# Optimization experiments

Hardware: AMD Instinct MI355X
Metric: run time of the kernel (lower is better)

The kernel has to match this reference:

```python
import jax, jax.numpy as jnp
import numpy as np

PF = 57     # player_features
TL = 35     # team_length (hardcoded in call)
EXTRA = 6   # trailing features x[:, :, 206:]
B, T = 64, 1024
D_IN = TL + 3 * PF + EXTRA          # 212
FEAT = 5 + 3 * 10 + EXTRA           # 41 (team_embed 5 + player_embed 30 + extra)
H = 256                             # LSTM units


def setup_inputs() -> dict:
    key = jax.random.key(0)
    ks = jax.random.split(key, 24)
    w = lambda k, shp, s=0.05: (jax.random.normal(k, shp, jnp.float32) * s)
    z = lambda n: jnp.zeros((n,), jnp.float32)
    return {
        "x": jax.random.normal(ks[0], (B, T, D_IN), jnp.float32),
        # encoder_player: Dense(57->27, relu), Dense(27->10, relu)
        "pe_w1": w(ks[1], (PF, 27)), "pe_b1": z(27),
        "pe_w2": w(ks[2], (27, 10)), "pe_b2": z(10),
        # encoder_team: Dense(35->17, relu), Dense(17->5, relu)
        "te_w1": w(ks[3], (TL, 17)), "te_b1": z(17),
        "te_w2": w(ks[4], (17, 5)),  "te_b2": z(5),
        # stacked LSTMs (keras kernel layout [in,4H] gate order i,f,c,o)
        "W1": w(ks[5], (FEAT, 4 * H)), "U1": w(ks[6], (H, 4 * H)), "bl1": z(4 * H),
        "W2": w(ks[7], (H, 4 * H)),    "U2": w(ks[8], (H, 4 * H)), "bl2": z(4 * H),
        "W3": w(ks[9], (H, 4 * H)),    "U3": w(ks[10], (H, 4 * H)), "bl3": z(4 * H),
        # head: Dense(256->100 relu), Dense(100->40 relu), Dense(40->2 softmax)
        "d1w": w(ks[11], (H, 100)), "d1b": z(100),
        "d2w": w(ks[12], (100, 40)), "d2b": z(40),
        "d3w": w(ks[13], (40, 2)),  "d3b": z(2),
    }


def _lstm_softmax(x, W, U, b):
    """Keras LSTM with activation=softmax, recurrent_activation=sigmoid.
    x: [B,T,D] -> hidden sequence [B,T,H]."""
    xz = jnp.einsum('btd,dk->btk', x, W) + b          # precompute input projection [B,T,4H]
    h0 = jnp.zeros((x.shape[0], U.shape[0]), x.dtype)

    def step(carry, xt):
        h, c = carry
        zt = xt + h @ U                               # [B,4H]
        i, f, g, o = jnp.split(zt, 4, axis=-1)        # keras gate order i,f,c,o
        c = jax.nn.sigmoid(f) * c + jax.nn.sigmoid(i) * jax.nn.softmax(g, axis=-1)
        h = jax.nn.sigmoid(o) * jax.nn.softmax(c, axis=-1)
        return (h, c), h

    _, hs = jax.lax.scan(step, (h0, h0), jnp.swapaxes(xz, 0, 1))
    return jnp.swapaxes(hs, 0, 1)


def reference(x, pe_w1, pe_b1, pe_w2, pe_b2, te_w1, te_b1, te_w2, te_b2,
              W1, U1, bl1, W2, U2, bl2, W3, U3, bl3,
              d1w, d1b, d2w, d2b, d3w, d3b):
    Bn, Tn = x.shape[0], x.shape[1]
    relu = jax.nn.relu

    # team encoder
    team = x[:, :, :TL].reshape(-1, TL)
    te = relu(relu(team @ te_w1 + te_b1) @ te_w2 + te_b2).reshape(Bn, Tn, -1)  # [B,T,5]

    # player encoder: shooter/assister/blocker rows concatenated then re-flattened
    s = x[:, :, TL:TL + PF].reshape(-1, PF)
    a = x[:, :, TL + PF:TL + 2 * PF].reshape(-1, PF)
    bk = x[:, :, TL + 2 * PF:TL + 3 * PF].reshape(-1, PF)
    players = jnp.concatenate([s, a, bk], axis=1).reshape(-1, PF)              # [3BT,57]
    pe = relu(relu(players @ pe_w1 + pe_b1) @ pe_w2 + pe_b2).reshape(Bn, Tn, -1)  # [B,T,30]

    # faithful out-of-range slices (clamp like TF strided_slice):
    shooter_e = pe[:, :, :PF]                  # whole 30 dims
    assister_e = pe[:, :, PF:2 * PF]           # empty [B,T,0]
    blocker_e = pe[:, :, 2 * PF:]              # empty [B,T,0]

    feat = jnp.concatenate(
        [te, shooter_e, assister_e, blocker_e, x[:, :, TL + 3 * PF:]], axis=2)  # [B,T,41]

    h = _lstm_softmax(feat, W1, U1, bl1)
    h = _lstm_softmax(h, W2, U2, bl2)
    h_last = _lstm_softmax(h, W3, U3, bl3)[:, -1]                               # [B,256]

    out = relu(h_last @ d1w + d1b)
    out = relu(out @ d2w + d2b)
    return jax.nn.softmax(out @ d3w + d3b, axis=-1)                             # [B,2]
```

## Files before the change

kernel.cpp:

```cpp
#include <hip/hip_runtime.h>

typedef _Float16 f16;
typedef _Float16 h2 __attribute__((ext_vector_type(2)));
typedef float f32x2 __attribute__((ext_vector_type(2)));

#define NBATCH 64
#define TSTEPS 1024
#define NH 256
#define FSTR 44

#define OFF_FEAT 0ull
#define OFF_XZ   11534336ull
#define OFF_H    145752064ull
#define OFF_UPK  179306496ull

#define QLDS 18
#define QALL 32
#define QSTR (QALL - QLDS)
#define SMEM_SCAN8 (QLDS * 1024 * 8 + 1024 + 4096 + 64)

__device__ __forceinline__ float sigmf(float z) {
  return 1.f / (1.f + __expf(-z));
}

__device__ __forceinline__ float wave_sum64(float v) {
#pragma unroll
  for (int off = 32; off; off >>= 1) v += __shfl_xor(v, off);
  return v;
}

__device__ __forceinline__ void fp8x4_mac(unsigned w, float4 hv,
                                          float& a0, float& a1) {
  f32x2 lo = __builtin_amdgcn_cvt_pk_f32_fp8(w, false);
  f32x2 hi = __builtin_amdgcn_cvt_pk_f32_fp8(w, true);
  a0 = fmaf(lo.x, hv.x, a0);
  a1 = fmaf(lo.y, hv.y, a1);
  a0 = fmaf(hi.x, hv.z, a0);
  a1 = fmaf(hi.y, hv.w, a1);
}

__global__ __launch_bounds__(256) void cvt_u_fp8(const float* __restrict__ U,
                                                 uint2* __restrict__ dst) {
  int id = blockIdx.x * 256 + threadIdx.x;
  int q = id >> 10, c = id & 1023;
  unsigned vx = 0, vy = 0;
  vx = __builtin_amdgcn_cvt_pk_fp8_f32(U[(8 * q + 0) * 1024 + c],
                                       U[(8 * q + 1) * 1024 + c], vx, false);
  vx = __builtin_amdgcn_cvt_pk_fp8_f32(U[(8 * q + 2) * 1024 + c],
                                       U[(8 * q + 3) * 1024 + c], vx, true);
  vy = __builtin_amdgcn_cvt_pk_fp8_f32(U[(8 * q + 4) * 1024 + c],
                                       U[(8 * q + 5) * 1024 + c], vy, false);
  vy = __builtin_amdgcn_cvt_pk_fp8_f32(U[(8 * q + 6) * 1024 + c],
                                       U[(8 * q + 7) * 1024 + c], vy, true);
  dst[id] = uint2{vx, vy};
}

__global__ __launch_bounds__(256) void embed_feat(
    const float* __restrict__ x,
    const float* __restrict__ pe_w1, const float* __restrict__ pe_b1,
    const float* __restrict__ pe_w2, const float* __restrict__ pe_b2,
    const float* __restrict__ te_w1, const float* __restrict__ te_b1,
    const float* __restrict__ te_w2, const float* __restrict__ te_b2,
    float* __restrict__ feat) {
  __shared__ float w[2548];
  const int tid = threadIdx.x;
  for (int i = tid; i < 595; i += 256) w[i] = te_w1[i];
  for (int i = tid; i < 17; i += 256) w[595 + i] = te_b1[i];
  for (int i = tid; i < 85; i += 256) w[612 + i] = te_w2[i];
  for (int i = tid; i < 5; i += 256) w[697 + i] = te_b2[i];
  for (int i = tid; i < 1539; i += 256) w[702 + i] = pe_w1[i];
  for (int i = tid; i < 27; i += 256) w[2241 + i] = pe_b1[i];
  for (int i = tid; i < 270; i += 256) w[2268 + i] = pe_w2[i];
  for (int i = tid; i < 10; i += 256) w[2538 + i] = pe_b2[i];
  __syncthreads();

  int row = blockIdx.x * 256 + tid;
  const float* xr = x + (size_t)row * 212;
  float* fr = feat + (size_t)row * FSTR;

  {
    float h1[17];
#pragma unroll
    for (int h = 0; h < 17; ++h) h1[h] = w[595 + h];
    for (int k = 0; k < 35; ++k) {
      float xv = xr[k];
#pragma unroll
      for (int h = 0; h < 17; ++h) h1[h] += xv * w[k * 17 + h];
    }
#pragma unroll
    for (int h = 0; h < 17; ++h) h1[h] = fmaxf(h1[h], 0.f);
    float t2[5];
#pragma unroll
    for (int h = 0; h < 5; ++h) t2[h] = w[697 + h];
#pragma unroll
    for (int k = 0; k < 17; ++k) {
#pragma unroll
      for (int h = 0; h < 5; ++h) t2[h] += h1[k] * w[612 + k * 5 + h];
    }
#pragma unroll
    for (int h = 0; h < 5; ++h) fr[h] = fmaxf(t2[h], 0.f);
  }
  for (int p = 0; p < 3; ++p) {
    const float* xp = xr + 35 + 57 * p;
    float h1[27];
#pragma unroll
    for (int h = 0; h < 27; ++h) h1[h] = w[2241 + h];
    for (int k = 0; k < 57; ++k) {
      float xv = xp[k];
#pragma unroll
      for (int h = 0; h < 27; ++h) h1[h] += xv * w[702 + k * 27 + h];
    }
#pragma unroll
    for (int h = 0; h < 27; ++h) h1[h] = fmaxf(h1[h], 0.f);
    float t2[10];
#pragma unroll
    for (int h = 0; h < 10; ++h) t2[h] = w[2538 + h];
#pragma unroll
    for (int k = 0; k < 27; ++k) {
#pragma unroll
      for (int h = 0; h < 10; ++h) t2[h] += h1[k] * w[2268 + k * 10 + h];
    }
#pragma unroll
    for (int h = 0; h < 10; ++h) fr[5 + 10 * p + h] = fmaxf(t2[h], 0.f);
  }
#pragma unroll
  for (int e = 0; e < 6; ++e) fr[35 + e] = xr[206 + e];
}

__global__ __launch_bounds__(256) void gemm_feat(
    const float* __restrict__ feat, const float* __restrict__ W,
    const float* __restrict__ bias, f16* __restrict__ C) {
  __shared__ float Wl[41 * 256];
  __shared__ float fl[64 * FSTR];
  int m0 = blockIdx.x * 64, n0 = blockIdx.y * 256;
  int t = threadIdx.x;
  for (int r = 0; r < 41; ++r) Wl[r * 256 + t] = W[r * 1024 + n0 + t];
  for (int i = t; i < 64 * FSTR; i += 256) fl[i] = feat[(size_t)m0 * FSTR + i];
  __syncthreads();
  float bv = bias[n0 + t];
  for (int r = 0; r < 64; ++r) {
    float acc = bv;
#pragma unroll
    for (int k = 0; k < 41; ++k) acc += fl[r * FSTR + k] * Wl[k * 256 + t];
    C[(size_t)(m0 + r) * 1024 + n0 + t] = (f16)acc;
  }
}

__global__ __launch_bounds__(256) void gemm_h(
    const f16* __restrict__ A, const float* __restrict__ B,
    const float* __restrict__ bias, f16* __restrict__ C) {
  __shared__ float As[32][72];
  __shared__ float Bs[32][64];
  int m0 = blockIdx.x * 64, n0 = blockIdx.y * 64;
  int t = threadIdx.x;
  int tx = t & 15, ty = t >> 4;
  float acc[4][4];
#pragma unroll
  for (int i = 0; i < 4; ++i)
#pragma unroll
    for (int j = 0; j < 4; ++j) acc[i][j] = 0.f;

  float bcol[4];
#pragma unroll
  for (int j = 0; j < 4; ++j) bcol[j] = bias[n0 + tx * 4 + j];

  for (int k0 = 0; k0 < 256; k0 += 32) {
    {
      int r = t >> 2, kq = (t & 3) * 8;
      const f16* ap = A + (size_t)(m0 + r) * 256 + k0 + kq;
      float4 raw = *(const float4*)ap;
      const f16* hv = (const f16*)&raw;
#pragma unroll
      for (int q = 0; q < 8; ++q) As[kq + q][r] = (float)hv[q];
    }
    {
      int kr = t >> 3, nq = (t & 7) * 8;
      const float* bp = B + (size_t)(k0 + kr) * 1024 + n0 + nq;
      float4 b0 = *(const float4*)bp;
      float4 b1 = *(const float4*)(bp + 4);
      *(float4*)&Bs[kr][nq] = b0;
      *(float4*)&Bs[kr][nq + 4] = b1;
    }
    __syncthreads();
#pragma unroll
    for (int kk = 0; kk < 32; ++kk) {
      float4 av = *(const float4*)&As[kk][ty * 4];
      float4 bv = *(const float4*)&Bs[kk][tx * 4];
      const float* ap = (const float*)&av;
      const float* bp = (const float*)&bv;
#pragma unroll
      for (int i = 0; i < 4; ++i)
#pragma unroll
        for (int j = 0; j < 4; ++j) acc[i][j] += ap[i] * bp[j];
    }
    __syncthreads();
  }
#pragma unroll
  for (int i = 0; i < 4; ++i) {
    int row = m0 + ty * 4 + i;
    alignas(8) f16 ov[4];
#pragma unroll
    for (int j = 0; j < 4; ++j) ov[j] = (f16)(acc[i][j] + bcol[j]);
    *(uint2*)(C + (size_t)row * 1024 + n0 + tx * 4) = *(const uint2*)ov;
  }
}

__global__ __launch_bounds__(512) void lstm_scan_f8(
    const uint2* __restrict__ Wall,
    const f16* __restrict__ xz,
    f16* __restrict__ hseq) {
  extern __shared__ char smem[];
  uint2* wlds = (uint2*)smem;
  float* hstore = (float*)(smem + QLDS * 1024 * 8);
  float* arr = (float*)(smem + QLDS * 1024 * 8 + 1024);
  float* red = (float*)(smem + QLDS * 1024 * 8 + 1024 + 4096);

  const int bid = blockIdx.x;
  const int t = threadIdx.x;
  const bool lowhalf = (t < 256);
  const uint2* Wt = Wall + QLDS * 1024;
  const float4* hst4 = (const float4*)hstore;

  for (int i = t; i < QLDS * 1024; i += 512) wlds[i] = Wall[i];
  if (lowhalf) hstore[t] = 0.f;
  float creg = 0.f;
  __syncthreads();

#pragma unroll 1
  for (int step = 0; step < TSTEPS; ++step) {
    const f16* xzrow = xz + ((size_t)bid * TSTEPS + step) * 1024;
    float xza = (float)xzrow[t];
    float xzb = (float)xzrow[t + 512];

    float a0 = 0.f, a1 = 0.f, b0 = 0.f, b1 = 0.f;
#pragma unroll 4
    for (int q = 0; q < QLDS; ++q) {
      uint2 wa = wlds[q * 1024 + t];
      uint2 wb = wlds[q * 1024 + t + 512];
      float4 h0 = hst4[2 * q];
      float4 h1 = hst4[2 * q + 1];
      fp8x4_mac(wa.x, h0, a0, a1);
      fp8x4_mac(wa.y, h1, a0, a1);
      fp8x4_mac(wb.x, h0, b0, b1);
      fp8x4_mac(wb.y, h1, b0, b1);
    }
#pragma unroll 4
    for (int q = 0; q < QSTR; ++q) {
      uint2 wa = Wt[q * 1024 + t];
      uint2 wb = Wt[q * 1024 + t + 512];
      float4 h0 = hst4[2 * (QLDS + q)];
      float4 h1 = hst4[2 * (QLDS + q) + 1];
      fp8x4_mac(wa.x, h0, a0, a1);
      fp8x4_mac(wa.y, h1, a0, a1);
      fp8x4_mac(wb.x, h0, b0, b1);
      fp8x4_mac(wb.y, h1, b0, b1);
    }
    float za = xza + a0 + a1;
    float zb = xzb + b0 + b1;

    float sa = sigmf(za);
    float ab = lowhalf ? __expf(zb) : sigmf(zb);
    arr[t] = sa;
    arr[t + 512] = ab;

    if (lowhalf) {
      float gs = wave_sum64(ab);
      if ((t & 63) == 0) red[t >> 6] = gs;
    }
    __syncthreads();

    float ec = 0.f;
    if (lowhalf) {
      float gsum = red[0] + red[1] + red[2] + red[3];
      float smg = ab / gsum;
      creg = arr[256 + t] * creg + sa * smg;
      ec = __expf(creg);
      float cs = wave_sum64(ec);
      if ((t & 63) == 0) red[8 + (t >> 6)] = cs;
    }
    __syncthreads();

    if (lowhalf) {
      float csum = red[8] + red[9] + red[10] + red[11];
      float hv = arr[768 + t] * (ec / csum);
      hstore[t] = hv;
      hseq[((size_t)bid * TSTEPS + step) * NH + t] = (f16)hv;
    }
    __syncthreads();
  }
}

__global__ __launch_bounds__(128) void head_k(
    const f16* __restrict__ hseq,
    const float* __restrict__ d1w, const float* __restrict__ d1b,
    const float* __restrict__ d2w, const float* __restrict__ d2b,
    const float* __restrict__ d3w, const float* __restrict__ d3b,
    float* __restrict__ out) {
  __shared__ float hl[256], o1[100], o2[40];
  int b = blockIdx.x, t = threadIdx.x;
  const f16* hrow = hseq + ((size_t)b * TSTEPS + (TSTEPS - 1)) * NH;
  for (int i = t; i < 256; i += 128) hl[i] = (float)hrow[i];
  __syncthreads();
  if (t < 100) {
    float acc = d1b[t];
    for (int k = 0; k < 256; ++k) acc += hl[k] * d1w[k * 100 + t];
    o1[t] = fmaxf(acc, 0.f);
  }
  __syncthreads();
  if (t < 40) {
    float acc = d2b[t];
    for (int k = 0; k < 100; ++k) acc += o1[k] * d2w[k * 40 + t];
    o2[t] = fmaxf(acc, 0.f);
  }
  __syncthreads();
  if (t == 0) {
    float a0 = d3b[0], a1 = d3b[1];
    for (int k = 0; k < 40; ++k) {
      a0 += o2[k] * d3w[k * 2];
      a1 += o2[k] * d3w[k * 2 + 1];
    }
    float m = fmaxf(a0, a1);
    float e0 = __expf(a0 - m), e1 = __expf(a1 - m);
    float s = e0 + e1;
    out[b * 2] = e0 / s;
    out[b * 2 + 1] = e1 / s;
  }
}

extern "C" void kernel_launch(void* const* d_in, const int* in_sizes, int n_in,
                              void* d_out, int out_size, void* d_ws, size_t ws_size,
                              hipStream_t stream) {
  const float* x = (const float*)d_in[0];
  const float* pe_w1 = (const float*)d_in[1];
  const float* pe_b1 = (const float*)d_in[2];
  const float* pe_w2 = (const float*)d_in[3];
  const float* pe_b2 = (const float*)d_in[4];
  const float* te_w1 = (const float*)d_in[5];
  const float* te_b1 = (const float*)d_in[6];
  const float* te_w2 = (const float*)d_in[7];
  const float* te_b2 = (const float*)d_in[8];
  const float* W1 = (const float*)d_in[9];
  const float* U1 = (const float*)d_in[10];
  const float* bl1 = (const float*)d_in[11];
  const float* W2 = (const float*)d_in[12];
  const float* U2m = (const float*)d_in[13];
  const float* bl2 = (const float*)d_in[14];
  const float* W3 = (const float*)d_in[15];
  const float* U3 = (const float*)d_in[16];
  const float* bl3 = (const float*)d_in[17];
  const float* d1w = (const float*)d_in[18];
  const float* d1b = (const float*)d_in[19];
  const float* d2w = (const float*)d_in[20];
  const float* d2b = (const float*)d_in[21];
  const float* d3w = (const float*)d_in[22];
  const float* d3b = (const float*)d_in[23];
  float* out = (float*)d_out;

  char* ws = (char*)d_ws;
  float* feat = (float*)(ws + OFF_FEAT);
  f16* xzbuf = (f16*)(ws + OFF_XZ);
  f16* hseq = (f16*)(ws + OFF_H);
  uint2* upk = (uint2*)(ws + OFF_UPK);

  hipFuncSetAttribute((const void*)lstm_scan_f8,
                      hipFuncAttributeMaxDynamicSharedMemorySize, SMEM_SCAN8);

  const float* Us[3] = {U1, U2m, U3};
  for (int l = 0; l < 3; ++l)
    cvt_u_fp8<<<128, 256, 0, stream>>>(Us[l], upk + (size_t)l * 32768);

  embed_feat<<<256, 256, 0, stream>>>(x, pe_w1, pe_b1, pe_w2, pe_b2,
                                      te_w1, te_b1, te_w2, te_b2, feat);
  gemm_feat<<<dim3(1024, 4), 256, 0, stream>>>(feat, W1, bl1, xzbuf);
  lstm_scan_f8<<<64, 512, SMEM_SCAN8, stream>>>(upk, xzbuf, hseq);

  gemm_h<<<dim3(1024, 16), 256, 0, stream>>>(hseq, W2, bl2, xzbuf);
  lstm_scan_f8<<<64, 512, SMEM_SCAN8, stream>>>(upk + 32768, xzbuf, hseq);

  gemm_h<<<dim3(1024, 16), 256, 0, stream>>>(hseq, W3, bl3, xzbuf);
  lstm_scan_f8<<<64, 512, SMEM_SCAN8, stream>>>(upk + 2 * 32768, xzbuf, hseq);

  head_k<<<64, 128, 0, stream>>>(hseq, d1w, d1b, d2w, d2b, d3w, d3b, out);
}
```

Baseline: 14.68 ms.

## Keep streamed weight slice in registers and do cell update in one wave

The 14 fp8 weight quads that were re-read from global memory every timestep are now loaded once into registers before the scan loop. The softmax/cell/hidden update is moved into a single wave of 64 threads, each handling 4 units. That wave does its reductions with shuffles only, which removes the cross-wave LDS reduction and one block barrier per step. The cost is higher register pressure (28 uint2 per thread) and serial work concentrated in one wave while the others sit idle at the barrier.

```diff
diff --git a/kernel.cpp b/kernel.cpp
--- a/kernel.cpp
+++ b/kernel.cpp
@@ -16,8 +16,8 @@
 
 #define QLDS 18
 #define QALL 32
-#define QSTR (QALL - QLDS)
-#define SMEM_SCAN8 (QLDS * 1024 * 8 + 1024 + 4096 + 64)
+#define QREG (QALL - QLDS)
+#define SMEM_SCAN8 (QLDS * 1024 * 8 + 1024 + 4096)
 
 __device__ __forceinline__ float sigmf(float z) {
   return 1.f / (1.f + __expf(-z));
@@ -205,6 +205,19 @@
   }
 }
 
+#define REGDECL(i) uint2 wr##i##a, wr##i##b;
+#define REGLOAD(i)                                \
+  wr##i##a = Wt[(i) * 1024 + t];                  \
+  wr##i##b = Wt[(i) * 1024 + t + 512];
+#define DOREG(i) {                                \
+    float4 h0 = hst4[2 * (QLDS + (i))];           \
+    float4 h1 = hst4[2 * (QLDS + (i)) + 1];       \
+    fp8x4_mac(wr##i##a.x, h0, a0, a1);            \
+    fp8x4_mac(wr##i##a.y, h1, a0, a1);            \
+    fp8x4_mac(wr##i##b.x, h0, b0, b1);            \
+    fp8x4_mac(wr##i##b.y, h1, b0, b1);            \
+  }
+
 __global__ __launch_bounds__(512) void lstm_scan_f8(
     const uint2* __restrict__ Wall,
     const f16* __restrict__ xz,
@@ -213,17 +226,22 @@
   uint2* wlds = (uint2*)smem;
   float* hstore = (float*)(smem + QLDS * 1024 * 8);
   float* arr = (float*)(smem + QLDS * 1024 * 8 + 1024);
-  float* red = (float*)(smem + QLDS * 1024 * 8 + 1024 + 4096);
 
   const int bid = blockIdx.x;
   const int t = threadIdx.x;
   const bool lowhalf = (t < 256);
   const uint2* Wt = Wall + QLDS * 1024;
   const float4* hst4 = (const float4*)hstore;
+  const float4* arr4 = (const float4*)arr;
+
+  REGDECL(0) REGDECL(1) REGDECL(2) REGDECL(3) REGDECL(4) REGDECL(5) REGDECL(6)
+  REGDECL(7) REGDECL(8) REGDECL(9) REGDECL(10) REGDECL(11) REGDECL(12) REGDECL(13)
+  REGLOAD(0) REGLOAD(1) REGLOAD(2) REGLOAD(3) REGLOAD(4) REGLOAD(5) REGLOAD(6)
+  REGLOAD(7) REGLOAD(8) REGLOAD(9) REGLOAD(10) REGLOAD(11) REGLOAD(12) REGLOAD(13)
 
   for (int i = t; i < QLDS * 1024; i += 512) wlds[i] = Wall[i];
-  if (lowhalf) hstore[t] = 0.f;
-  float creg = 0.f;
+  if (t < 256) hstore[t] = 0.f;
+  float c0 = 0.f, c1 = 0.f, c2 = 0.f, c3 = 0.f;
   __syncthreads();
 
 #pragma unroll 1
@@ -244,47 +262,38 @@
       fp8x4_mac(wb.x, h0, b0, b1);
       fp8x4_mac(wb.y, h1, b0, b1);
     }
-#pragma unroll 4
-    for (int q = 0; q < QSTR; ++q) {
-      uint2 wa = Wt[q * 1024 + t];
-      uint2 wb = Wt[q * 1024 + t + 512];
-      float4 h0 = hst4[2 * (QLDS + q)];
-      float4 h1 = hst4[2 * (QLDS + q) + 1];
-      fp8x4_mac(wa.x, h0, a0, a1);
-      fp8x4_mac(wa.y, h1, a0, a1);
-      fp8x4_mac(wb.x, h0, b0, b1);
-      fp8x4_mac(wb.y, h1, b0, b1);
-    }
+    DOREG(0) DOREG(1) DOREG(2) DOREG(3) DOREG(4) DOREG(5) DOREG(6)
+    DOREG(7) DOREG(8) DOREG(9) DOREG(10) DOREG(11) DOREG(12) DOREG(13)
+
     float za = xza + a0 + a1;
     float zb = xzb + b0 + b1;
 
     float sa = sigmf(za);
     float ab = lowhalf ? __expf(zb) : sigmf(zb);
     arr[t] = sa;
-    arr[t + 512] = ab;
-
-    if (lowhalf) {
-      float gs = wave_sum64(ab);
-      if ((t & 63) == 0) red[t >> 6] = gs;
-    }
+    arr[512 + t] = ab;
     __syncthreads();
 
-    float ec = 0.f;
-    if (lowhalf) {
-      float gsum = red[0] + red[1] + red[2] + red[3];
-      float smg = ab / gsum;
-      creg = arr[256 + t] * creg + sa * smg;
-      ec = __expf(creg);
-      float cs = wave_sum64(ec);
-      if ((t & 63) == 0) red[8 + (t >> 6)] = cs;
-    }
-    __syncthreads();
-
-    if (lowhalf) {
-      float csum = red[8] + red[9] + red[10] + red[11];
-      float hv = arr[768 + t] * (ec / csum);
-      hstore[t] = hv;
-      hseq[((size_t)bid * TSTEPS + step) * NH + t] = (f16)hv;
+    if (t < 64) {
+      float4 iv = arr4[t];
+      float4 fv = arr4[64 + t];
+      float4 gv = arr4[128 + t];
+      float4 ov = arr4[192 + t];
+      float gs = wave_sum64(gv.x + gv.y + gv.z + gv.w);
+      float ginv = 1.f / gs;
+      c0 = fmaf(fv.x, c0, iv.x * gv.x * ginv);
+      c1 = fmaf(fv.y, c1, iv.y * gv.y * ginv);
+      c2 = fmaf(fv.z, c2, iv.z * gv.z * ginv);
+      c3 = fmaf(fv.w, c3, iv.w * gv.w * ginv);
+      float e0 = __expf(c0), e1 = __expf(c1), e2 = __expf(c2), e3 = __expf(c3);
+      float cs = wave_sum64(e0 + e1 + e2 + e3);
+      float cinv = 1.f / cs;
+      float h0 = ov.x * e0 * cinv, h1 = ov.y * e1 * cinv;
+      float h2v = ov.z * e2 * cinv, h3 = ov.w * e3 * cinv;
+      ((float4*)hstore)[t] = float4{h0, h1, h2v, h3};
+      alignas(8) f16 hv4[4] = {(f16)h0, (f16)h1, (f16)h2v, (f16)h3};
+      *(uint2*)(hseq + ((size_t)bid * TSTEPS + step) * NH + 4 * t) =
+          *(const uint2*)hv4;
     }
     __syncthreads();
   }
```

Result: slower. 28.70 ms (+95.5%).
